# Kernel tuning notes

Measured on AMD Instinct MI355X. Metric: run time of the kernel, lower is better.

Reference implementation:

```python
import jax, jax.numpy as jnp
from jax import lax
import numpy as np
import math

IMG_H, IMG_W = 592, 800  # stride-16 image for a 50x37 feature map


def _make_anchors(fx=50, fy=37, base=8, dsr=16):
    rows = []
    for x in range(fx):
        for y in range(fy):
            for size in [base, 2 * base, 4 * base]:
                rows.append([(x - size / 2) * dsr, (y - size / 2) * dsr,
                             (x + size / 2) * dsr, (y + size / 2) * dsr])
                s = math.sqrt(size ** 2 / 2)
                rows.append([(x - s) * dsr, (y - s / 2) * dsr, (x + s) * dsr, (y + s / 2) * dsr])
                rows.append([(x - s / 2) * dsr, (y - s) * dsr, (x + s / 2) * dsr, (y + s) * dsr])
    return np.array(rows, np.float32)


def setup_inputs() -> dict:
    key = jax.random.key(0)
    k = jax.random.split(key, 8)
    B, G, H, W = 32, 20, 50, 37
    feats = jax.random.normal(k[0], (B, 512, H, W), jnp.float32)
    a = _make_anchors()
    keep = (a[:, 0] >= 0) & (a[:, 1] >= 0) & (a[:, 2] <= IMG_W) & (a[:, 3] <= IMG_H)
    idxs_inside = jnp.asarray(np.nonzero(keep)[0].astype(np.int32))
    anchors = jnp.asarray(a[keep])
    # valid xyxy GT boxes inside the image
    x1 = jax.random.uniform(k[1], (B, G)) * (IMG_W - 160)
    y1 = jax.random.uniform(k[2], (B, G)) * (IMG_H - 160)
    w = 32.0 + jax.random.uniform(k[3], (B, G)) * 96.0
    h = 32.0 + jax.random.uniform(k[4], (B, G)) * 96.0
    gt_boxes = jnp.stack([x1, y1, x1 + w, y1 + h], -1)
    W3 = jax.random.normal(k[5], (512, 512, 3, 3), jnp.float32) * 0.02
    b3 = jnp.zeros((512,), jnp.float32)
    Wcls = jax.random.normal(k[6], (18, 512, 1, 1), jnp.float32) * 0.02
    bcls = jnp.zeros((18,), jnp.float32)
    Wloc = jax.random.normal(k[7], (36, 512, 1, 1), jnp.float32) * 0.02
    bloc = jnp.zeros((36,), jnp.float32)
    return {"feats": feats, "gt_boxes": gt_boxes, "anchors": anchors,
            "W3": W3, "b3": b3, "Wcls": Wcls, "bcls": bcls,
            "Wloc": Wloc, "bloc": bloc, "idxs_inside": idxs_inside}


def _conv(x, w, b, pad):
    y = lax.conv_general_dilated(x, w, (1, 1), pad,
                                 dimension_numbers=("NCHW", "OIHW", "NCHW"))
    return y + b[None, :, None, None]


def reference(feats, gt_boxes, anchors, W3, b3, Wcls, bcls, Wloc, bloc, idxs_inside):
    B = feats.shape[0]
    rpn_conv1 = jax.nn.relu(_conv(feats, W3, b3, "SAME"))
    cls_score = _conv(rpn_conv1, Wcls, bcls, "VALID")          # [B,18,H,W]
    _, C, H, Wd = cls_score.shape
    logits = cls_score.reshape(B, 2, (C * H) // 2, Wd)          # reshape(x, 2)
    prob = jax.nn.softmax(logits, axis=1)
    prob_back = prob.reshape(B, C, H, Wd)                       # reshape back to 18
    loc_pred = _conv(rpn_conv1, Wloc, bloc, "VALID")            # [B,36,H,W]

    # select inside-image anchors
    logits_sel = logits.transpose(0, 2, 3, 1).reshape(B, -1, 2)[:, idxs_inside, :]
    loc_sel = loc_pred.transpose(0, 2, 3, 1).reshape(B, -1, 4)[:, idxs_inside, :]

    # vectorized anchors x gt IoU (replaces the triple python loop)
    ix1 = jnp.maximum(anchors[None, :, None, 0], gt_boxes[:, None, :, 0])
    iy1 = jnp.maximum(anchors[None, :, None, 1], gt_boxes[:, None, :, 1])
    ix2 = jnp.minimum(anchors[None, :, None, 2], gt_boxes[:, None, :, 2])
    iy2 = jnp.minimum(anchors[None, :, None, 3], gt_boxes[:, None, :, 3])
    inter = jnp.clip(ix2 - ix1, 0) * jnp.clip(iy2 - iy1, 0)     # [B,A,G]
    area_a = (anchors[:, 2] - anchors[:, 0]) * (anchors[:, 3] - anchors[:, 1])
    area_g = (gt_boxes[..., 2] - gt_boxes[..., 0]) * (gt_boxes[..., 3] - gt_boxes[..., 1])
    iou = inter / jnp.maximum(area_a[None, :, None] + area_g[:, None, :] - inter, 1e-8)

    max_iou = iou.max(-1)                                       # [B,A]
    matched = iou.argmax(-1)                                    # [B,A] gt index per anchor
    gt_best = iou.argmax(1)                                     # [B,G] best anchor per gt
    A = anchors.shape[0]
    is_best = jnp.zeros((B, A), bool).at[jnp.arange(B)[:, None], gt_best].set(True)
    labels = (is_best | (max_iou > 0.7)).astype(jnp.int32)      # positives=1, rest 0

    logsm = jax.nn.log_softmax(logits_sel, -1)
    loss_cls = -jnp.take_along_axis(logsm, labels[..., None], -1).mean()

    tgt = jnp.take_along_axis(gt_boxes, matched[:, :, None], axis=1)  # [B,A,4]
    d = loc_sel - tgt
    sl1 = jnp.where(jnp.abs(d) < 1.0, 0.5 * d * d, jnp.abs(d) - 0.5)
    loss_loc = (sl1 * labels[..., None].astype(sl1.dtype)).sum() / 256.0

    return prob_back, loc_pred, loss_cls, loss_loc
```

## Files before the change

kernel.cpp:

```cpp
#include <hip/hip_runtime.h>
#include <stdint.h>

typedef unsigned short u16;
typedef unsigned int   u32;
typedef unsigned long long u64;

typedef __bf16 v8bf __attribute__((ext_vector_type(8)));
typedef float  v4f  __attribute__((ext_vector_type(4)));

#define NBATCH 32
#define NCH    512
#define FH     50
#define FW     37
#define PIX    1850
#define MTOT   59200
#define KTOT   4608
#define HP     52
#define WP     39
#define NG     20
#define W3N    (NCH*KTOT)
#define WCBN   (64*512)
#define BORDN  364544
#define NT     72

#define PROB_N 1065600
#define LC_IDX 3196800
#define LL_IDX 3196801

__device__ __forceinline__ u16 f2bf(float f) {
    u32 u = __float_as_uint(f);
    u += 0x7fffu + ((u >> 16) & 1u);
    return (u16)(u >> 16);
}

__device__ __forceinline__ void gl_lds16(const u16* g, u16* l) {
    __builtin_amdgcn_global_load_lds((const __attribute__((address_space(1))) u32*)g,
                                     (__attribute__((address_space(3))) u32*)l,
                                     16, 0, 0);
}

__device__ __forceinline__ int offA_of(int T, int kh) {
    const int dydx = T >> 3;
    const int ci0  = (T & 7) << 6;
    return ((dydx / 3) * WP + (dydx % 3)) * NCH + ci0 + kh * 32;
}

__global__ __launch_bounds__(256) void pad_kernel(const float* __restrict__ feats,
                                                  u16* __restrict__ fpad) {
    __shared__ float t[64][65];
    const int b  = blockIdx.z;
    const int c0 = blockIdx.y * 64;
    const int p0 = blockIdx.x * 64;
    const int tid = threadIdx.x;
    {
        const int cl = tid >> 2, seg = tid & 3;
        const float* src = feats + ((size_t)b * NCH + c0 + cl) * PIX;
        const int pbase = p0 + seg * 16;
        #pragma unroll
        for (int i = 0; i < 16; i++) {
            int p = pbase + i;
            t[cl][seg * 16 + i] = (p < PIX) ? src[p] : 0.f;
        }
    }
    __syncthreads();
    {
        const int pl = tid >> 2, cs = tid & 3;
        const int p = p0 + pl;
        if (p < PIX) {
            const int h = p / FW, w = p % FW;
            size_t dst = (((size_t)b * HP + h + 1) * WP + (w + 1)) * NCH + c0 + cs * 16;
            u32 pk[8];
            #pragma unroll
            for (int i = 0; i < 8; i++) {
                u32 lo = f2bf(t[cs * 16 + 2 * i][pl]);
                u32 hi = f2bf(t[cs * 16 + 2 * i + 1][pl]);
                pk[i] = lo | (hi << 16);
            }
            *(uint4*)&fpad[dst]     = make_uint4(pk[0], pk[1], pk[2], pk[3]);
            *(uint4*)&fpad[dst + 8] = make_uint4(pk[4], pk[5], pk[6], pk[7]);
        }
    }
}

__global__ void prep_kernel(const float* __restrict__ w3, const float* __restrict__ wcls,
                            const float* __restrict__ wloc,
                            u16* __restrict__ wbt, u16* __restrict__ wcb,
                            u16* __restrict__ fpad, float* __restrict__ out) {
    int t = blockIdx.x * 256 + threadIdx.x;
    if (t < 2) out[LC_IDX + t] = 0.f;
    if (t < W3N) {
        int co = t / KTOT, k = t % KTOT;
        int dydx = k >> 9, ci = k & 511;
        wbt[t] = f2bf(w3[((size_t)co * NCH + ci) * 9 + dydx]);
    } else if (t < W3N + WCBN) {
        int t2 = t - W3N;
        int c = t2 >> 9, ci = t2 & 511;
        float v = (c < 18) ? wcls[c * 512 + ci]
                : (c < 54) ? wloc[(c - 18) * 512 + ci] : 0.f;
        wcb[t2] = f2bf(v);
    } else if (t < W3N + WCBN + BORDN) {
        int t3 = t - (W3N + WCBN);
        int c8 = t3 & 63;
        int pi = (t3 >> 6) % 178;
        int b  = (t3 >> 6) / 178;
        int h, w;
        if (pi < 39)       { h = 0;        w = pi; }
        else if (pi < 78)  { h = 51;       w = pi - 39; }
        else if (pi < 128) { h = pi - 77;  w = 0; }
        else               { h = pi - 127; w = 38; }
        size_t dst = (((size_t)b * HP + h) * WP + w) * NCH + c8 * 8;
        *(uint4*)&fpad[dst] = make_uint4(0, 0, 0, 0);
    }
}

__global__ __launch_bounds__(512, 2) void conv3x3_mfma(const u16* __restrict__ fpad,
                                                       const u16* __restrict__ wbt,
                                                       const float* __restrict__ b3,
                                                       u16* __restrict__ conv1) {
    __shared__ __align__(16) u16 As[2][2][256][32];
    __shared__ __align__(16) u16 Bs[2][2][256][32];

    const int wg     = ((int)blockIdx.x & 7) * 58 + ((int)blockIdx.x >> 3);
    const int n_base = (wg & 1) * 256;
    const int m_base = (wg >> 1) * 256;

    const int tid = threadIdx.x;
    const int w   = tid >> 6;
    const int l   = tid & 63;

    const int sr   = l >> 2;
    const int sseg = (l & 3) ^ ((l >> 3) & 3);
    int rbA[2], rbB[2];
    #pragma unroll
    for (int c = 0; c < 2; c++) {
        const int r  = w * 32 + c * 16 + sr;
        const int m  = m_base + r;
        const int mm = (m < MTOT) ? m : 0;
        const int b = mm / PIX, p = mm % PIX;
        const int y = p / FW, x = p % FW;
        rbA[c] = ((b * HP + y) * WP + x) * NCH + sseg * 8;
        rbB[c] = (n_base + r) * KTOT + sseg * 8;
    }
    u16* const aBase = &As[0][0][0][0] + w * 1024;
    u16* const bBase = &Bs[0][0][0][0] + w * 1024;

    const int wm = w >> 2, wn = w & 3;
    const int lm = l & 15, quad = l >> 4;
    const int psw = (quad ^ ((lm >> 1) & 3)) * 8;
    const u16* const aR = &As[0][0][0][0] + (wm * 128 + lm) * 32 + psw;
    const u16* const bR = &Bs[0][0][0][0] + (wn * 64  + lm) * 32 + psw;

    v4f acc[8][4];
    #pragma unroll
    for (int i = 0; i < 8; i++)
        #pragma unroll
        for (int j = 0; j < 4; j++)
            #pragma unroll
            for (int r = 0; r < 4; r++) acc[i][j][r] = 0.f;

    v8bf afA[4], afB[4], bf0[4], bf1[4];

#define STAGE_A(buf, kh, Tp) { \
        const int oA_ = offA_of((Tp), (kh)); \
        u16* const dA_ = aBase + (buf) * 16384 + (kh) * 8192; \
        gl_lds16(fpad + rbA[0] + oA_, dA_); \
        gl_lds16(fpad + rbA[1] + oA_, dA_ + 512); }
#define STAGE_B(buf, kh, Tp) { \
        const int oB_ = (Tp) * 64 + (kh) * 32; \
        u16* const dB_ = bBase + (buf) * 16384 + (kh) * 8192; \
        gl_lds16(wbt + rbB[0] + oB_, dB_); \
        gl_lds16(wbt + rbB[1] + oB_, dB_ + 512); }
#define RD_A(dst, buf, kh, mh) { \
        _Pragma("unroll") \
        for (int i_ = 0; i_ < 4; i_++) \
            dst[i_] = *(const v8bf*)(aR + (buf) * 16384 + (kh) * 8192 + ((mh) * 4 + i_) * 512); }
#define RD_B(dst, buf, kh) { \
        _Pragma("unroll") \
        for (int j_ = 0; j_ < 4; j_++) \
            dst[j_] = *(const v8bf*)(bR + (buf) * 16384 + (kh) * 8192 + j_ * 512); }
#define MM(afv, bfv, mh) { \
        __builtin_amdgcn_s_setprio(1); \
        _Pragma("unroll") \
        for (int i_ = 0; i_ < 4; i_++) \
            _Pragma("unroll") \
            for (int j_ = 0; j_ < 4; j_++) \
                acc[(mh) * 4 + i_][j_] = __builtin_amdgcn_mfma_f32_16x16x32_bf16( \
                    afv[i_], bfv[j_], acc[(mh) * 4 + i_][j_], 0, 0, 0); \
        __builtin_amdgcn_s_setprio(0); }

    STAGE_A(0, 0, 0); STAGE_B(0, 0, 0);
    STAGE_A(0, 1, 0); STAGE_B(0, 1, 0);
    STAGE_A(1, 0, 1); STAGE_B(1, 0, 1);
    asm volatile("s_waitcnt vmcnt(4)" ::: "memory");
    __builtin_amdgcn_s_barrier();
    RD_A(afA, 0, 0, 0); RD_B(bf0, 0, 0);

    for (int T = 0; T < NT; ++T) {
        const int cb = T & 1;
        const int nb = cb ^ 1;
        RD_A(afB, cb, 0, 1);
        if (T + 1 < NT) STAGE_A(nb, 1, T + 1);
        __builtin_amdgcn_s_barrier();
        MM(afA, bf0, 0);
        if (T < NT - 1) { asm volatile("s_waitcnt vmcnt(6)" ::: "memory"); }
        else            { asm volatile("s_waitcnt vmcnt(0)" ::: "memory"); }
        __builtin_amdgcn_s_barrier();
        RD_A(afA, cb, 1, 0);
        RD_B(bf1, cb, 1);
        if (T + 1 < NT) STAGE_B(nb, 1, T + 1);
        __builtin_amdgcn_s_barrier();
        MM(afB, bf0, 1);
        __builtin_amdgcn_s_barrier();
        RD_A(afB, cb, 1, 1);
        if (T + 2 < NT) STAGE_A(cb, 0, T + 2);
        __builtin_amdgcn_s_barrier();
        MM(afA, bf1, 0);
        if (T < NT - 2)       { asm volatile("s_waitcnt vmcnt(6)" ::: "memory"); }
        else if (T == NT - 2) { asm volatile("s_waitcnt vmcnt(4)" ::: "memory"); }
        else                  { asm volatile("s_waitcnt vmcnt(0)" ::: "memory"); }
        __builtin_amdgcn_s_barrier();
        if (T + 1 < NT) { RD_A(afA, nb, 0, 0); RD_B(bf0, nb, 0); }
        if (T + 2 < NT) STAGE_B(cb, 0, T + 2);
        __builtin_amdgcn_s_barrier();
        MM(afB, bf1, 1);
        __builtin_amdgcn_s_barrier();
    }
#undef MM
#undef RD_B
#undef RD_A
#undef STAGE_B
#undef STAGE_A

    #pragma unroll
    for (int nj = 0; nj < 4; nj++) {
        const int n = n_base + wn * 64 + nj * 16 + lm;
        const float bias = b3[n];
        #pragma unroll
        for (int i = 0; i < 8; i++) {
            #pragma unroll
            for (int r = 0; r < 4; r++) {
                const int m = m_base + wm * 128 + i * 16 + quad * 4 + r;
                if (m < MTOT) {
                    float v = acc[i][nj][r] + bias;
                    v = v > 0.f ? v : 0.f;
                    conv1[(size_t)m * NCH + n] = f2bf(v);
                }
            }
        }
    }
}

__global__ __launch_bounds__(256) void head_mfma(const u16* __restrict__ conv1,
                                                 const u16* __restrict__ wcb,
                                                 const float* __restrict__ bcls,
                                                 const float* __restrict__ bloc,
                                                 float* __restrict__ out) {
    __shared__ __align__(16) u16 As[128][64];
    __shared__ __align__(16) u16 Bs[64][64];
    __shared__ float ct[128][66];

    const int tid = threadIdx.x;
    const int m_base = blockIdx.x * 128;
    const int wave = tid >> 6;
    const int lane = tid & 63;
    const int srow  = tid >> 3;
    const int seg_g = (tid & 7) ^ (srow & 7);

    int rbA[4];
    #pragma unroll
    for (int r = 0; r < 4; r++) {
        int m = m_base + r * 32 + srow;
        int mm = (m < MTOT) ? m : 0;
        rbA[r] = mm * NCH + seg_g * 8;
    }
    int rbB[2];
    #pragma unroll
    for (int r = 0; r < 2; r++)
        rbB[r] = (r * 32 + srow) * NCH + seg_g * 8;

    u16* const asb = &As[0][0] + wave * 512;
    u16* const bsb = &Bs[0][0] + wave * 512;

    const int wn = wave * 16;
    const int lm = lane & 15;
    const int quad = lane >> 4;
    const int x7 = lm & 7;

    v4f acc[8];
    #pragma unroll
    for (int i = 0; i < 8; i++)
        #pragma unroll
        for (int r = 0; r < 4; r++) acc[i][r] = 0.f;

    for (int k0 = 0; k0 < NCH; k0 += 64) {
        #pragma unroll
        for (int r = 0; r < 4; r++)
            gl_lds16(conv1 + rbA[r] + k0, asb + r * 2048);
        #pragma unroll
        for (int r = 0; r < 2; r++)
            gl_lds16(wcb + rbB[r] + k0, bsb + r * 2048);
        __syncthreads();

        #pragma unroll
        for (int kh = 0; kh < 2; kh++) {
            const int ps = (((kh << 2) | quad) ^ x7) * 8;
            v8bf bf = *(const v8bf*)(&Bs[0][0] + (wn + lm) * 64 + ps);
            #pragma unroll
            for (int i = 0; i < 8; i++) {
                v8bf af = *(const v8bf*)(&As[0][0] + (i * 16 + lm) * 64 + ps);
                acc[i] = __builtin_amdgcn_mfma_f32_16x16x32_bf16(af, bf, acc[i], 0, 0, 0);
            }
        }
        __syncthreads();
    }

    const int col = wn + lm;
    const float bias = (col < 18) ? bcls[col] : (col < 54) ? bloc[col - 18] : 0.f;
    #pragma unroll
    for (int i = 0; i < 8; i++)
        #pragma unroll
        for (int r = 0; r < 4; r++)
            ct[i * 16 + quad * 4 + r][col] = acc[i][r] + bias;
    __syncthreads();

    const int c = tid >> 2;
    const int pix4 = tid & 3;
    for (int px = pix4; px < 128; px += 4) {
        const int m = m_base + px;
        if (m >= MTOT) break;
        const int b = m / PIX;
        const int p = m - b * PIX;
        if (c < 9) {
            float s0 = ct[px][c], s1 = ct[px][c + 9];
            float mx = fmaxf(s0, s1);
            float e0 = __expf(s0 - mx), e1 = __expf(s1 - mx);
            float inv = 1.f / (e0 + e1);
            out[((size_t)b * 18 + c) * PIX + p]     = e0 * inv;
            out[((size_t)b * 18 + c + 9) * PIX + p] = e1 * inv;
        } else if (c >= 18 && c < 54) {
            out[(size_t)PROB_N + ((size_t)b * 36 + (c - 18)) * PIX + p] = ct[px][c];
        }
    }
}

__global__ __launch_bounds__(256) void iouloss_kernel(const float* __restrict__ anchors,
                                                      const float* __restrict__ gtb,
                                                      const int* __restrict__ idxs,
                                                      int A,
                                                      const float* __restrict__ outr,
                                                      float* __restrict__ out) {
    __shared__ float g[NG * 4];
    __shared__ u64 keys[NG];
    __shared__ int gbest[NG];
    __shared__ float red[8];
    const int b = blockIdx.y;
    const int tid = threadIdx.x;
    if (tid < NG * 4) g[tid] = gtb[b * NG * 4 + tid];
    if (tid < NG) keys[tid] = 0ull;
    __syncthreads();

    u64 lk[NG];
    #pragma unroll
    for (int gi = 0; gi < NG; gi++) lk[gi] = 0ull;
    for (int a = tid; a < A; a += 256) {
        const float ax1 = anchors[a * 4 + 0], ay1 = anchors[a * 4 + 1];
        const float ax2 = anchors[a * 4 + 2], ay2 = anchors[a * 4 + 3];
        const float areaA = (ax2 - ax1) * (ay2 - ay1);
        const u64 atag = (u64)(0xFFFFFFFFu - (u32)a);
        #pragma unroll
        for (int gi = 0; gi < NG; gi++) {
            float gx1 = g[gi*4], gy1 = g[gi*4+1], gx2 = g[gi*4+2], gy2 = g[gi*4+3];
            float iw = fmaxf(fminf(ax2, gx2) - fmaxf(ax1, gx1), 0.f);
            float ih = fmaxf(fminf(ay2, gy2) - fmaxf(ay1, gy1), 0.f);
            float inter = iw * ih;
            float areaG = (gx2 - gx1) * (gy2 - gy1);
            float iou = inter / fmaxf(areaA + areaG - inter, 1e-8f);
            u64 key = (((u64)__float_as_uint(iou)) << 32) | atag;
            if (key > lk[gi]) lk[gi] = key;
        }
    }
    #pragma unroll
    for (int gi = 0; gi < NG; gi++) {
        u64 k = lk[gi];
        #pragma unroll
        for (int off = 32; off; off >>= 1) {
            u64 o = __shfl_xor(k, off);
            k = (o > k) ? o : k;
        }
        if ((tid & 63) == 0) atomicMax(&keys[gi], k);
    }
    __syncthreads();
    if (tid < NG) gbest[tid] = (int)(0xFFFFFFFFu - (u32)(keys[tid] & 0xFFFFFFFFull));
    __syncthreads();

    float lc = 0.f, ll = 0.f;
    for (int a = tid; a < A; a += 256) {
        const float ax1 = anchors[a * 4 + 0], ay1 = anchors[a * 4 + 1];
        const float ax2 = anchors[a * 4 + 2], ay2 = anchors[a * 4 + 3];
        const float areaA = (ax2 - ax1) * (ay2 - ay1);
        float best = -1.f;
        int bg = 0;
        #pragma unroll
        for (int gi = 0; gi < NG; gi++) {
            float gx1 = g[gi*4], gy1 = g[gi*4+1], gx2 = g[gi*4+2], gy2 = g[gi*4+3];
            float iw = fmaxf(fminf(ax2, gx2) - fmaxf(ax1, gx1), 0.f);
            float ih = fmaxf(fminf(ay2, gy2) - fmaxf(ay1, gy1), 0.f);
            float inter = iw * ih;
            float areaG = (gx2 - gx1) * (gy2 - gy1);
            float iou = inter / fmaxf(areaA + areaG - inter, 1e-8f);
            if (iou > best) { best = iou; bg = gi; }
        }
        int lbl = (best > 0.7f) ? 1 : 0;
        if (!lbl) {
            #pragma unroll
            for (int gi = 0; gi < NG; gi++) lbl |= (gbest[gi] == a);
        }
        const int idx = idxs[a];
        const int cpr = idx / PIX;
        const int rem = idx % PIX;
        float p0 = outr[((size_t)b * 18 + cpr) * PIX + rem];
        float p1 = outr[((size_t)b * 18 + cpr + 9) * PIX + rem];
        lc += -logf(lbl ? p1 : p0);
        if (lbl) {
            const int hh = idx / 333;
            const int r2 = idx % 333;
            const int ww = r2 / 9;
            const int c4 = r2 % 9;
            const int pp = hh * FW + ww;
            #pragma unroll
            for (int t = 0; t < 4; t++) {
                float lv = outr[(size_t)PROB_N + ((size_t)b * 36 + c4 * 4 + t) * PIX + pp];
                float d = lv - g[bg * 4 + t];
                float ad = fabsf(d);
                ll += (ad < 1.f) ? 0.5f * d * d : ad - 0.5f;
            }
        }
    }
    #pragma unroll
    for (int off = 32; off; off >>= 1) {
        lc += __shfl_xor(lc, off);
        ll += __shfl_xor(ll, off);
    }
    const int lane = tid & 63, wave = tid >> 6;
    if (lane == 0) { red[wave] = lc; red[4 + wave] = ll; }
    __syncthreads();
    if (tid == 0) {
        float slc = red[0] + red[1] + red[2] + red[3];
        float sll = red[4] + red[5] + red[6] + red[7];
        atomicAdd(&out[LC_IDX], slc * (1.f / (32.f * (float)A)));
        atomicAdd(&out[LL_IDX], sll * (1.f / 256.f));
    }
}

extern "C" void kernel_launch(void* const* d_in, const int* in_sizes, int n_in,
                              void* d_out, int out_size, void* d_ws, size_t ws_size,
                              hipStream_t stream) {
    const float* feats   = (const float*)d_in[0];
    const float* gtb     = (const float*)d_in[1];
    const float* anchors = (const float*)d_in[2];
    const float* W3      = (const float*)d_in[3];
    const float* b3      = (const float*)d_in[4];
    const float* Wcls    = (const float*)d_in[5];
    const float* bcls    = (const float*)d_in[6];
    const float* Wloc    = (const float*)d_in[7];
    const float* bloc    = (const float*)d_in[8];
    const int*   idxs    = (const int*)d_in[9];
    const int A = in_sizes[9];
    float* out = (float*)d_out;

    char* ws = (char*)d_ws;
    size_t off = 0;
    auto alloc = [&](size_t bytes) -> void* {
        void* p = ws + off;
        off = (off + bytes + 255) & ~(size_t)255;
        return p;
    };
    const size_t fpad_n = (size_t)NBATCH * HP * WP * NCH;
    u16* fpad   = (u16*)alloc(fpad_n * 2);
    u16* wbt    = (u16*)alloc((size_t)W3N * 2);
    u16* wcb    = (u16*)alloc((size_t)WCBN * 2);
    u16* conv1  = (u16*)alloc((size_t)MTOT * NCH * 2);

    const int prep_tot = W3N + WCBN + BORDN;
    prep_kernel<<<(prep_tot + 255) / 256, 256, 0, stream>>>(W3, Wcls, Wloc, wbt, wcb, fpad, out);
    pad_kernel<<<dim3(29, 8, NBATCH), 256, 0, stream>>>(feats, fpad);
    conv3x3_mfma<<<464, 512, 0, stream>>>(fpad, wbt, b3, conv1);
    head_mfma<<<463, 256, 0, stream>>>(conv1, wcb, bcls, bloc, out);
    iouloss_kernel<<<dim3(1, NBATCH), 256, 0, stream>>>(anchors, gtb, idxs, A, out, out);
}
```

Before: 781.3 us.

## Replace fine-grained interleaved GEMM pipeline with simple double-buffered loop

Replaces the hand-interleaved schedule, which staged half-tiles and overlapped LDS reads with MFMA across many barriers and partial vmcnt waits, with a plain double buffer. Each iteration now waits for all loads, issues the next tile's global-to-LDS loads, reads all fragments, then runs the MFMAs. It also drops the s_setprio hints around the MFMA blocks. This lowers barrier count and schedule complexity, but it exposes load latency through the full vmcnt(0) wait and raises register pressure from holding six fragment arrays at once.

```diff
diff --git a/kernel.cpp b/kernel.cpp
--- a/kernel.cpp
+++ b/kernel.cpp
@@ -158,8 +158,6 @@
             #pragma unroll
             for (int r = 0; r < 4; r++) acc[i][j][r] = 0.f;
 
-    v8bf afA[4], afB[4], bf0[4], bf1[4];
-
 #define STAGE_A(buf, kh, Tp) { \
         const int oA_ = offA_of((Tp), (kh)); \
         u16* const dA_ = aBase + (buf) * 16384 + (kh) * 8192; \
@@ -179,51 +177,32 @@
         for (int j_ = 0; j_ < 4; j_++) \
             dst[j_] = *(const v8bf*)(bR + (buf) * 16384 + (kh) * 8192 + j_ * 512); }
 #define MM(afv, bfv, mh) { \
-        __builtin_amdgcn_s_setprio(1); \
         _Pragma("unroll") \
         for (int i_ = 0; i_ < 4; i_++) \
             _Pragma("unroll") \
             for (int j_ = 0; j_ < 4; j_++) \
                 acc[(mh) * 4 + i_][j_] = __builtin_amdgcn_mfma_f32_16x16x32_bf16( \
-                    afv[i_], bfv[j_], acc[(mh) * 4 + i_][j_], 0, 0, 0); \
-        __builtin_amdgcn_s_setprio(0); }
+                    afv[i_], bfv[j_], acc[(mh) * 4 + i_][j_], 0, 0, 0); }
 
     STAGE_A(0, 0, 0); STAGE_B(0, 0, 0);
     STAGE_A(0, 1, 0); STAGE_B(0, 1, 0);
-    STAGE_A(1, 0, 1); STAGE_B(1, 0, 1);
-    asm volatile("s_waitcnt vmcnt(4)" ::: "memory");
-    __builtin_amdgcn_s_barrier();
-    RD_A(afA, 0, 0, 0); RD_B(bf0, 0, 0);
 
     for (int T = 0; T < NT; ++T) {
         const int cb = T & 1;
         const int nb = cb ^ 1;
-        RD_A(afB, cb, 0, 1);
-        if (T + 1 < NT) STAGE_A(nb, 1, T + 1);
+        asm volatile("s_waitcnt vmcnt(0)" ::: "memory");
         __builtin_amdgcn_s_barrier();
-        MM(afA, bf0, 0);
-        if (T < NT - 1) { asm volatile("s_waitcnt vmcnt(6)" ::: "memory"); }
-        else            { asm volatile("s_waitcnt vmcnt(0)" ::: "memory"); }
-        __builtin_amdgcn_s_barrier();
-        RD_A(afA, cb, 1, 0);
-        RD_B(bf1, cb, 1);
-        if (T + 1 < NT) STAGE_B(nb, 1, T + 1);
-        __builtin_amdgcn_s_barrier();
-        MM(afB, bf0, 1);
-        __builtin_amdgcn_s_barrier();
-        RD_A(afB, cb, 1, 1);
-        if (T + 2 < NT) STAGE_A(cb, 0, T + 2);
-        __builtin_amdgcn_s_barrier();
-        MM(afA, bf1, 0);
-        if (T < NT - 2)       { asm volatile("s_waitcnt vmcnt(6)" ::: "memory"); }
-        else if (T == NT - 2) { asm volatile("s_waitcnt vmcnt(4)" ::: "memory"); }
-        else                  { asm volatile("s_waitcnt vmcnt(0)" ::: "memory"); }
-        __builtin_amdgcn_s_barrier();
-        if (T + 1 < NT) { RD_A(afA, nb, 0, 0); RD_B(bf0, nb, 0); }
-        if (T + 2 < NT) STAGE_B(cb, 0, T + 2);
-        __builtin_amdgcn_s_barrier();
-        MM(afB, bf1, 1);
-        __builtin_amdgcn_s_barrier();
+        if (T + 1 < NT) {
+            STAGE_A(nb, 0, T + 1); STAGE_B(nb, 0, T + 1);
+            STAGE_A(nb, 1, T + 1); STAGE_B(nb, 1, T + 1);
+        }
+        v8bf b0[4], b1[4], a00[4], a01[4], a10[4], a11[4];
+        RD_B(b0, cb, 0); RD_A(a00, cb, 0, 0); RD_A(a01, cb, 0, 1);
+        RD_B(b1, cb, 1); RD_A(a10, cb, 1, 0); RD_A(a11, cb, 1, 1);
+        MM(a00, b0, 0);
+        MM(a01, b0, 1);
+        MM(a10, b1, 0);
+        MM(a11, b1, 1);
     }
 #undef MM
 #undef RD_B
```

New measurement: 819.1 us. +4.8%, slower.
